# Performance work log

Hardware: AMD Instinct MI355X
Metric: run time of the kernel (lower is better)

## Reference

```python
import jax, jax.numpy as jnp
from jax import lax
import numpy as np

MAX_POINTS = 100  # hardcoded pad size in _convert_diagram_to_tensor
MAX_DIM = 2


def setup_inputs() -> dict:
    key = jax.random.key(0)
    x = jax.random.normal(key, (16, 2048, 3), dtype=jnp.float32)
    # nn.Parameter(torch.linspace(0, max_edge_length, num_filtrations))
    filtration_values = jnp.linspace(0.0, 2.0, 50, dtype=jnp.float32)
    return {"x": x, "filtration_values": filtration_values}


def _pairwise_dist(x):
    # [B,N,N] Euclidean distances via GEMM (avoids [B,N,N,F] blowup)
    sq = jnp.sum(x * x, axis=-1)  # [B,N]
    d2 = sq[:, :, None] + sq[:, None, :] - 2.0 * jnp.einsum("bnf,bmf->bnm", x, x)
    return jnp.sqrt(jnp.maximum(d2, 0.0))


def _mst_deaths(D):
    # Prim's algorithm on a single [N,N] distance matrix.
    # The N-1 MST edge weights are exactly the H0 death times of the
    # Vietoris-Rips filtration (births are all 0).
    N = D.shape[0]
    inf = jnp.array(np.inf, D.dtype)
    in_tree = jnp.zeros((N,), bool).at[0].set(True)
    min_dist = D[0]

    def step(carry, _):
        in_tree, min_dist = carry
        md = jnp.where(in_tree, inf, min_dist)
        j = jnp.argmin(md)
        w = md[j]
        in_tree = in_tree.at[j].set(True)
        min_dist = jnp.minimum(min_dist, D[j])
        return (in_tree, min_dist), w

    _, deaths = lax.scan(step, (in_tree, min_dist), None, length=N - 1)
    return deaths  # [N-1]


def reference(x, filtration_values):
    B, N, _ = x.shape
    D = _pairwise_dist(x)                      # [B,N,N]
    deaths = jax.vmap(_mst_deaths)(D)          # [B,N-1] finite H0 deaths

    # Persistence diagrams: H0 points (0, death), sorted by persistence
    # (= death, since births are 0) descending, top MAX_POINTS, zero-padded.
    top_deaths, _ = lax.top_k(deaths, MAX_POINTS)      # [B,100]
    d0 = jnp.stack([jnp.zeros_like(top_deaths), top_deaths], axis=-1)  # [B,100,2]
    zero_dgm = jnp.zeros_like(d0)
    # H1/H2 of a Rips complex require full matrix reduction; gudhi computes
    # them on CPU. This reference covers H0 exactly and pads H1/H2 with zeros.
    diagrams = jnp.stack([d0, zero_dgm, zero_dgm], axis=1)  # [B,3,100,2]

    # Betti-0 curve: #components at eps = N - #(MST edges with weight <= eps)
    n_merged = jnp.sum(deaths[:, :, None] <= filtration_values[None, None, :], axis=1)
    betti0 = (N - n_merged).astype(jnp.float32)             # [B,F]
    zero_curve = jnp.zeros_like(betti0)
    betti_curves = jnp.stack([betti0, zero_curve, zero_curve], axis=1)  # [B,3,F]

    return diagrams, betti_curves
```

## Files before the change

kernel.cpp:

```cpp
#include <hip/hip_runtime.h>
#include <math.h>


#define PH_N   2048
#define PH_B   16
#define PH_F   50
#define MAXPTS 100
#define ROUNDS 11
#define RB     16
#define RPB    (PH_N / RB)
#define KA_TPB 256
#define JPL    32

typedef unsigned long long u64;
typedef unsigned int u32;

__device__ __forceinline__ float sq3(float x, float y, float z) {
    return __fadd_rn(__fadd_rn(__fmul_rn(x, x), __fmul_rn(y, y)), __fmul_rn(z, z));
}
__device__ __forceinline__ float d2f(float px, float py, float pz, float ps,
                                     float qx, float qy, float qz, float qs) {
    float dot = __fadd_rn(__fadd_rn(__fmul_rn(px, qx), __fmul_rn(py, qy)),
                          __fmul_rn(pz, qz));
    return __fsub_rn(__fadd_rn(ps, qs), __fmul_rn(2.0f, dot));
}

template<int CTRL>
__device__ __forceinline__ float dpp_min(float v) {
    int vi = __float_as_int(v);
    int sh = __builtin_amdgcn_update_dpp(vi, vi, CTRL, 0xF, 0xF, false);
    return fminf(v, __int_as_float(sh));
}
template<int CTRL>
__device__ __forceinline__ int dpp_imin(int v) {
    int sh = __builtin_amdgcn_update_dpp(v, v, CTRL, 0xF, 0xF, false);
    return min(v, sh);
}

__global__ void k_init(int* __restrict__ comp, u64* __restrict__ compBest,
                       int* __restrict__ cnt) {
    const int b = blockIdx.x, tid = threadIdx.x;
    for (int i = tid; i < PH_N; i += blockDim.x) {
        comp[b * PH_N + i]     = i;
        compBest[b * PH_N + i] = ~0ULL;
    }
    if (tid == 0) cnt[b] = 0;
}

__global__ __launch_bounds__(KA_TPB, 1)
void k_best(const float* __restrict__ x, const int* __restrict__ comp,
            u64* __restrict__ compBest) {
    __shared__ float4 spts[PH_N];
    __shared__ int    scomp[PH_N];
    __shared__ u64    sbest[PH_N];

    const int b = blockIdx.y, rb = blockIdx.x, tid = threadIdx.x;
    const int lane = tid & 63, wave = tid >> 6;
    const float* xb = x + (size_t)b * PH_N * 3;

    for (int i = tid; i < PH_N; i += KA_TPB) scomp[i] = comp[b * PH_N + i];
    __syncthreads();
    {
        int c0 = scomp[0], diff = 0;
        for (int i = tid; i < PH_N; i += KA_TPB) diff |= (scomp[i] != c0);
        if (!__syncthreads_or(diff)) return;
    }

    for (int i = tid; i < PH_N; i += KA_TPB) {
        float px = xb[3 * i], py = xb[3 * i + 1], pz = xb[3 * i + 2];
        spts[i]  = make_float4(px, py, pz, sq3(px, py, pz));
        sbest[i] = ~0ULL;
    }
    __syncthreads();

    float xj[JPL], yj[JPL], zj[JPL], sj[JPL];
    int   cj[JPL];
    #pragma unroll
    for (int k = 0; k < JPL; ++k) {
        float4 qv = spts[lane + (k << 6)];
        xj[k] = qv.x; yj[k] = qv.y; zj[k] = qv.z; sj[k] = qv.w;
        cj[k] = scomp[lane + (k << 6)];
    }

    const float INF = __builtin_inff();
    for (int r = wave; r < RPB; r += KA_TPB / 64) {
        const int    i  = rb * RPB + r;
        const int    ci = scomp[i];
        const float4 pi = spts[i];
        float m[JPL]; int ix[JPL];
        #pragma unroll
        for (int k = 0; k < JPL; ++k) {
            float d2 = d2f(pi.x, pi.y, pi.z, pi.w, xj[k], yj[k], zj[k], sj[k]);
            d2   = fmaxf(d2, 0.0f);
            m[k] = (cj[k] == ci) ? INF : d2;
            ix[k] = k;
        }
        #pragma unroll
        for (int s = JPL / 2; s > 0; s >>= 1) {
            #pragma unroll
            for (int k = 0; k < s; ++k)
                if (m[k + s] < m[k]) { m[k] = m[k + s]; ix[k] = ix[k + s]; }
        }
        const float vl = m[0];
        float w = vl;
        w = dpp_min<0x111>(w); w = dpp_min<0x112>(w); w = dpp_min<0x114>(w);
        w = dpp_min<0x118>(w); w = dpp_min<0x142>(w); w = dpp_min<0x143>(w);
        const float wm =
            __int_as_float(__builtin_amdgcn_readlane(__float_as_int(w), 63));
        if (wm < INF) {
            int jw = lane + (ix[0] << 6);
            int jc = (vl == wm) ? jw : 0x7FFFFFFF;
            jc = dpp_imin<0x111>(jc); jc = dpp_imin<0x112>(jc);
            jc = dpp_imin<0x114>(jc); jc = dpp_imin<0x118>(jc);
            jc = dpp_imin<0x142>(jc); jc = dpp_imin<0x143>(jc);
            const int j = __builtin_amdgcn_readlane(jc, 63);
            if (lane == 0) {
                int a = min(i, j), c2 = max(i, j);
                u64 key = ((u64)__float_as_uint(wm) << 22) | ((u64)a << 11) | (u64)c2;
                atomicMin(&sbest[ci], key);
            }
        }
    }
    __syncthreads();
    for (int c = tid; c < PH_N; c += KA_TPB) {
        u64 k = sbest[c];
        if (k != ~0ULL) atomicMin(&compBest[(size_t)b * PH_N + c], k);
    }
}

__global__ __launch_bounds__(1024)
void k_merge(u64* __restrict__ compBest, int* __restrict__ comp,
             float* __restrict__ deathsD2, int* __restrict__ cnt) {
    __shared__ u64 scb[PH_N];
    __shared__ int scm[PH_N];
    __shared__ int sp[PH_N];
    __shared__ int sq_[PH_N];
    const int b = blockIdx.x, tid = threadIdx.x, T = 1024;
    u64* cb = compBest + (size_t)b * PH_N;
    int* cm = comp + (size_t)b * PH_N;

    int any = 0;
    for (int i = tid; i < PH_N; i += T) {
        u64 k = cb[i];
        scb[i] = k; scm[i] = cm[i];
        any |= (k != ~0ULL);
    }
    if (!__syncthreads_or(any)) return;

    for (int c = tid; c < PH_N; c += T) {
        u64 k = scb[c];
        int pp = c;
        if (k != ~0ULL) {
            int a = (int)((k >> 11) & 0x7FF), d = (int)(k & 0x7FF);
            int ca = scm[a], cd = scm[d];
            pp = (ca == c) ? cd : ca;
        }
        sp[c] = pp;
    }
    __syncthreads();
    for (int c = tid; c < PH_N; c += T) {
        u64 k = scb[c];
        if (k != ~0ULL) {
            int tc = sp[c];
            bool mutual = (sp[tc] == c);
            if (!mutual || c < tc) {
                int slot = atomicAdd(&cnt[b], 1);
                deathsD2[(size_t)b * PH_N + slot] = __uint_as_float((u32)(k >> 22));
            }
        }
    }
    __syncthreads();
    for (int c = tid; c < PH_N; c += T) {
        u64 k = scb[c];
        if (k != ~0ULL) {
            int tc = sp[c];
            if (sp[tc] == c && c < tc) sp[c] = c;
        }
    }
    __syncthreads();
    int* cur = sp; int* nxt = sq_;
    for (int it = 0; it < 12; ++it) {
        int changed = 0;
        for (int c = tid; c < PH_N; c += T) {
            int v = cur[cur[c]];
            nxt[c] = v;
            changed |= (v != cur[c]);
        }
        int* t = cur; cur = nxt; nxt = t;
        if (!__syncthreads_or(changed)) break;
    }
    for (int v = tid; v < PH_N; v += T) cm[v] = cur[scm[v]];
    for (int c = tid; c < PH_N; c += T) cb[c] = ~0ULL;
}

__global__ __launch_bounds__(1024)
void k_final(const float* __restrict__ deathsD2, const float* __restrict__ filt,
             float* __restrict__ out) {
    __shared__ float deaths[PH_N];
    __shared__ int   scnt[PH_F];
    const int b = blockIdx.x, tid = threadIdx.x, T = 1024;
    const float INF = __builtin_inff();

    for (int t = tid; t < PH_N; t += T) {
        deaths[t] = (t < PH_N - 1)
                        ? sqrtf(deathsD2[(size_t)b * PH_N + t])
                        : -INF;
    }
    __syncthreads();

    for (int k = 2; k <= PH_N; k <<= 1) {
        for (int jj = k >> 1; jj > 0; jj >>= 1) {
            for (int i = tid; i < PH_N; i += T) {
                int ixj = i ^ jj;
                if (ixj > i) {
                    float a = deaths[i];
                    float c = deaths[ixj];
                    bool up = ((i & k) == 0);
                    if (up ? (a > c) : (a < c)) {
                        deaths[i]   = c;
                        deaths[ixj] = a;
                    }
                }
            }
            __syncthreads();
        }
    }

    if (tid < PH_F) {
        float eps = filt[tid];
        int lo = 0, hi = PH_N;
        while (lo < hi) {
            int mid = (lo + hi) >> 1;
            if (deaths[mid] <= eps) lo = mid + 1; else hi = mid;
        }
        scnt[tid] = lo - 1;
    }
    __syncthreads();

    float* dg = out + (size_t)b * (3 * MAXPTS * 2);
    for (int t = tid; t < 3 * MAXPTS * 2; t += T) {
        float val = 0.0f;
        if (t < 2 * MAXPTS && (t & 1)) {
            int k = t >> 1;
            val = deaths[PH_N - 1 - k];
        }
        dg[t] = val;
    }
    float* bc = out + (size_t)PH_B * (3 * MAXPTS * 2) + (size_t)b * (3 * PH_F);
    for (int t = tid; t < 3 * PH_F; t += T) {
        float val = 0.0f;
        if (t < PH_F) val = (float)(PH_N - scnt[t]);
        bc[t] = val;
    }
}

extern "C" void kernel_launch(void* const* d_in, const int* in_sizes, int n_in,
                              void* d_out, int out_size, void* d_ws, size_t ws_size,
                              hipStream_t stream) {
    const float* x    = (const float*)d_in[0];
    const float* filt = (const float*)d_in[1];
    float* out        = (float*)d_out;

    char* ws = (char*)d_ws;
    u64*   compBest = (u64*)ws;
    int*   comp     = (int*)(ws + (size_t)PH_B * PH_N * 8);
    float* dD2      = (float*)(comp + PH_B * PH_N);
    int*   cnt      = (int*)(dD2 + PH_B * PH_N);

    k_init<<<PH_B, 256, 0, stream>>>(comp, compBest, cnt);
    for (int r = 0; r < ROUNDS; ++r) {
        k_best<<<dim3(RB, PH_B), KA_TPB, 0, stream>>>(x, comp, compBest);
        k_merge<<<PH_B, 1024, 0, stream>>>(compBest, comp, dD2, cnt);
    }
    k_final<<<PH_B, 1024, 0, stream>>>(dD2, filt, out);
}
```

Measured before the change: 329.3 us.

## Fuse Boruvka merge into per-round best-edge kernel with double-buffered state

Folds the separate merge kernel into the best-edge kernel. Every block redundantly recomputes the component relabeling from the previous round's best edges, using ping-pong buffers and round tags in the key's upper bits, so no reset pass is needed. This cuts the launch count from 22 to 12 and removes the serialization between merge and search. In exchange, the merge work is repeated in all 16 row blocks per batch, and shared arrays shrink to 16-bit to make room.

Result: no change. 333.6 us (+1.3%).

```diff
diff --git a/kernel.cpp b/kernel.cpp
--- a/kernel.cpp
+++ b/kernel.cpp
@@ -9,11 +9,12 @@
 #define ROUNDS 11
 #define RB     16
 #define RPB    (PH_N / RB)
-#define KA_TPB 256
+#define TPB    256
 #define JPL    32
 
 typedef unsigned long long u64;
 typedef unsigned int u32;
+typedef unsigned short u16;
 
 __device__ __forceinline__ float sq3(float x, float y, float z) {
     return __fadd_rn(__fadd_rn(__fmul_rn(x, x), __fmul_rn(y, y)), __fmul_rn(z, z));
@@ -37,36 +38,106 @@
     return min(v, sh);
 }
 
-__global__ void k_init(int* __restrict__ comp, u64* __restrict__ compBest,
-                       int* __restrict__ cnt) {
-    const int b = blockIdx.x, tid = threadIdx.x;
-    for (int i = tid; i < PH_N; i += blockDim.x) {
-        comp[b * PH_N + i]     = i;
-        compBest[b * PH_N + i] = ~0ULL;
-    }
-    if (tid == 0) cnt[b] = 0;
-}
-
-__global__ __launch_bounds__(KA_TPB, 1)
-void k_best(const float* __restrict__ x, const int* __restrict__ comp,
-            u64* __restrict__ compBest) {
+__global__ void k_init(u64* __restrict__ cb, int* __restrict__ cnt) {
+    const size_t n = (size_t)2 * PH_B * PH_N;
+    for (size_t i = (size_t)blockIdx.x * blockDim.x + threadIdx.x; i < n;
+         i += (size_t)gridDim.x * blockDim.x)
+        cb[i] = ~0ULL;
+    if (blockIdx.x == 0 && threadIdx.x < PH_B) cnt[threadIdx.x] = 0;
+}
+
+__global__ __launch_bounds__(TPB, 1)
+void k_round(const float* __restrict__ x, u64* __restrict__ cb,
+             int* __restrict__ comp, float* __restrict__ dD2,
+             int* __restrict__ cnt, int r)
+{
     __shared__ float4 spts[PH_N];
-    __shared__ int    scomp[PH_N];
+    __shared__ u16    scomp[PH_N];
     __shared__ u64    sbest[PH_N];
-
-    const int b = blockIdx.y, rb = blockIdx.x, tid = threadIdx.x;
+    __shared__ u16    sp[PH_N];
+
+    const int rb = blockIdx.x, b = blockIdx.y, tid = threadIdx.x;
     const int lane = tid & 63, wave = tid >> 6;
+    const size_t bN = (size_t)b * PH_N;
+    const int par = r & 1;
+    u64* cbw = cb + (size_t)par * PH_B * PH_N + bN;
+    u64* cbr = cb + (size_t)(par ^ 1) * PH_B * PH_N + bN;
+    int* cmw = comp + (size_t)par * PH_B * PH_N + bN;
+    int* cmr = comp + (size_t)(par ^ 1) * PH_B * PH_N + bN;
     const float* xb = x + (size_t)b * PH_N * 3;
 
-    for (int i = tid; i < PH_N; i += KA_TPB) scomp[i] = comp[b * PH_N + i];
-    __syncthreads();
+    if (r == 0) { for (int i = tid; i < PH_N; i += TPB) scomp[i] = (u16)i; }
+    else        { for (int i = tid; i < PH_N; i += TPB) scomp[i] = (u16)cmr[i]; }
+    __syncthreads();
+
     {
         int c0 = scomp[0], diff = 0;
-        for (int i = tid; i < PH_N; i += KA_TPB) diff |= (scomp[i] != c0);
+        for (int i = tid; i < PH_N; i += TPB) diff |= (scomp[i] != c0);
+        if (!__syncthreads_or(diff)) {
+            if (rb == 0) for (int i = tid; i < PH_N; i += TPB) cmw[i] = scomp[i];
+            return;
+        }
+    }
+
+    if (r > 0) {
+        for (int c = tid; c < PH_N; c += TPB) sbest[c] = cbr[c];
+        __syncthreads();
+        const u32 mytag = (u32)(ROUNDS - (r - 1));
+        for (int c = tid; c < PH_N; c += TPB) {
+            u64 k = sbest[c];
+            int pp = c;
+            if ((u32)(k >> 54) == mytag) {
+                int a = (int)((k >> 11) & 0x7FF), d = (int)(k & 0x7FF);
+                int ca = scomp[a], cd = scomp[d];
+                pp = (ca == c) ? cd : ca;
+            }
+            sp[c] = (u16)pp;
+        }
+        __syncthreads();
+        if (rb == 0) {
+            for (int c = tid; c < PH_N; c += TPB) {
+                u64 k = sbest[c];
+                if ((u32)(k >> 54) == mytag) {
+                    int tc = sp[c];
+                    bool mutual = (sp[tc] == c);
+                    if (!mutual || c < tc) {
+                        int slot = atomicAdd(&cnt[b], 1);
+                        dD2[bN + slot] =
+                            __uint_as_float((u32)((k >> 22) & 0xFFFFFFFFu));
+                    }
+                }
+            }
+        }
+        __syncthreads();
+        for (int c = tid; c < PH_N; c += TPB) {
+            u64 k = sbest[c];
+            if ((u32)(k >> 54) == mytag) {
+                int tc = sp[c];
+                if (sp[tc] == c && c < tc) sp[c] = (u16)c;
+            }
+        }
+        __syncthreads();
+        for (int it = 0; it < 12; ++it) {
+            int changed = 0;
+            for (int c = tid; c < PH_N; c += TPB) {
+                u16 t = sp[sp[c]];
+                if (t != sp[c]) { sp[c] = t; changed = 1; }
+            }
+            if (!__syncthreads_or(changed)) break;
+        }
+        for (int v = tid; v < PH_N; v += TPB) scomp[v] = sp[scomp[v]];
+        __syncthreads();
+    }
+
+    if (rb == 0) for (int i = tid; i < PH_N; i += TPB) cmw[i] = scomp[i];
+    {
+        int c0 = scomp[0], diff = 0;
+        for (int i = tid; i < PH_N; i += TPB) diff |= (scomp[i] != c0);
         if (!__syncthreads_or(diff)) return;
     }
-
-    for (int i = tid; i < PH_N; i += KA_TPB) {
+    if (r == ROUNDS) return;
+
+    for (int i = tid; i < PH_N; i += TPB) {
         float px = xb[3 * i], py = xb[3 * i + 1], pz = xb[3 * i + 2];
         spts[i]  = make_float4(px, py, pz, sq3(px, py, pz));
         sbest[i] = ~0ULL;
@@ -83,8 +154,9 @@
     }
 
     const float INF = __builtin_inff();
-    for (int r = wave; r < RPB; r += KA_TPB / 64) {
-        const int    i  = rb * RPB + r;
+    const u64 tagbits = (u64)(ROUNDS - r) << 54;
+    for (int rr = wave; rr < RPB; rr += TPB / 64) {
+        const int    i  = rb * RPB + rr;
         const int    ci = scomp[i];
         const float4 pi = spts[i];
         float m[JPL]; int ix[JPL];
@@ -116,81 +188,17 @@
             const int j = __builtin_amdgcn_readlane(jc, 63);
             if (lane == 0) {
                 int a = min(i, j), c2 = max(i, j);
-                u64 key = ((u64)__float_as_uint(wm) << 22) | ((u64)a << 11) | (u64)c2;
+                u64 key = tagbits | ((u64)__float_as_uint(wm) << 22) |
+                          ((u64)a << 11) | (u64)c2;
                 atomicMin(&sbest[ci], key);
             }
         }
     }
     __syncthreads();
-    for (int c = tid; c < PH_N; c += KA_TPB) {
+    for (int c = tid; c < PH_N; c += TPB) {
         u64 k = sbest[c];
-        if (k != ~0ULL) atomicMin(&compBest[(size_t)b * PH_N + c], k);
-    }
-}
-
-__global__ __launch_bounds__(1024)
-void k_merge(u64* __restrict__ compBest, int* __restrict__ comp,
-             float* __restrict__ deathsD2, int* __restrict__ cnt) {
-    __shared__ u64 scb[PH_N];
-    __shared__ int scm[PH_N];
-    __shared__ int sp[PH_N];
-    __shared__ int sq_[PH_N];
-    const int b = blockIdx.x, tid = threadIdx.x, T = 1024;
-    u64* cb = compBest + (size_t)b * PH_N;
-    int* cm = comp + (size_t)b * PH_N;
-
-    int any = 0;
-    for (int i = tid; i < PH_N; i += T) {
-        u64 k = cb[i];
-        scb[i] = k; scm[i] = cm[i];
-        any |= (k != ~0ULL);
-    }
-    if (!__syncthreads_or(any)) return;
-
-    for (int c = tid; c < PH_N; c += T) {
-        u64 k = scb[c];
-        int pp = c;
-        if (k != ~0ULL) {
-            int a = (int)((k >> 11) & 0x7FF), d = (int)(k & 0x7FF);
-            int ca = scm[a], cd = scm[d];
-            pp = (ca == c) ? cd : ca;
-        }
-        sp[c] = pp;
-    }
-    __syncthreads();
-    for (int c = tid; c < PH_N; c += T) {
-        u64 k = scb[c];
-        if (k != ~0ULL) {
-            int tc = sp[c];
-            bool mutual = (sp[tc] == c);
-            if (!mutual || c < tc) {
-                int slot = atomicAdd(&cnt[b], 1);
-                deathsD2[(size_t)b * PH_N + slot] = __uint_as_float((u32)(k >> 22));
-            }
-        }
-    }
-    __syncthreads();
-    for (int c = tid; c < PH_N; c += T) {
-        u64 k = scb[c];
-        if (k != ~0ULL) {
-            int tc = sp[c];
-            if (sp[tc] == c && c < tc) sp[c] = c;
-        }
-    }
-    __syncthreads();
-    int* cur = sp; int* nxt = sq_;
-    for (int it = 0; it < 12; ++it) {
-        int changed = 0;
-        for (int c = tid; c < PH_N; c += T) {
-            int v = cur[cur[c]];
-            nxt[c] = v;
-            changed |= (v != cur[c]);
-        }
-        int* t = cur; cur = nxt; nxt = t;
-        if (!__syncthreads_or(changed)) break;
-    }
-    for (int v = tid; v < PH_N; v += T) cm[v] = cur[scm[v]];
-    for (int c = tid; c < PH_N; c += T) cb[c] = ~0ULL;
+        if (k != ~0ULL) atomicMin(&cbw[c], k);
+    }
 }
 
 __global__ __launch_bounds__(1024)
@@ -262,15 +270,13 @@
     float* out        = (float*)d_out;
 
     char* ws = (char*)d_ws;
-    u64*   compBest = (u64*)ws;
-    int*   comp     = (int*)(ws + (size_t)PH_B * PH_N * 8);
-    float* dD2      = (float*)(comp + PH_B * PH_N);
-    int*   cnt      = (int*)(dD2 + PH_B * PH_N);
-
-    k_init<<<PH_B, 256, 0, stream>>>(comp, compBest, cnt);
-    for (int r = 0; r < ROUNDS; ++r) {
-        k_best<<<dim3(RB, PH_B), KA_TPB, 0, stream>>>(x, comp, compBest);
-        k_merge<<<PH_B, 1024, 0, stream>>>(compBest, comp, dD2, cnt);
-    }
+    u64*   cbB  = (u64*)ws;
+    int*   comp = (int*)(ws + (size_t)2 * PH_B * PH_N * 8);
+    float* dD2  = (float*)(comp + 2 * PH_B * PH_N);
+    int*   cnt  = (int*)(dD2 + PH_B * PH_N);
+
+    k_init<<<64, 256, 0, stream>>>(cbB, cnt);
+    for (int r = 0; r <= ROUNDS; ++r)
+        k_round<<<dim3(RB, PH_B), TPB, 0, stream>>>(x, cbB, comp, dD2, cnt, r);
     k_final<<<PH_B, 1024, 0, stream>>>(dD2, filt, out);
 }
```
